# Kernel tuning notes

Hardware: AMD Instinct MI355X
Metric: run time of the kernel (lower is better)

Reference implementation:

```python
import jax, jax.numpy as jnp
import numpy as np

N, E, G = 100000, 1600000, 256      # nodes, edges, graphs in batch
IN_C, HID, OUT_C = 4, 128, 120
ALPHA = 0.5


def setup_inputs() -> dict:
    key = jax.random.key(0)
    ks = jax.random.split(key, 12)
    def w(k, i, o):
        return jax.random.normal(k, (i, o), jnp.float32) / np.float32(np.sqrt(i))
    return {
        "x": jax.random.normal(ks[0], (N, IN_C), jnp.float32),
        "edge_index": jax.random.randint(ks[1], (2, E), 0, N),
        "batch_seg": jnp.sort(jax.random.randint(ks[2], (N,), 0, G)),
        # DirGNNConv holds two independent GCNConvs (in / reversed direction)
        "W_in": w(ks[3], IN_C, HID),  "b_in": jnp.zeros((HID,), jnp.float32),
        "W_in_r": w(ks[4], IN_C, HID), "b_in_r": jnp.zeros((HID,), jnp.float32),
        "W_mid": w(ks[5], HID, HID),  "b_mid": jnp.zeros((HID,), jnp.float32),
        "W_mid_r": w(ks[6], HID, HID), "b_mid_r": jnp.zeros((HID,), jnp.float32),
        "W_out": w(ks[7], HID, OUT_C), "b_out": jnp.zeros((OUT_C,), jnp.float32),
        "W_out_r": w(ks[8], HID, OUT_C), "b_out_r": jnp.zeros((OUT_C,), jnp.float32),
    }


def _gcn(x, W, b, src, dst, n):
    # GCNConv with add_self_loops=False (DirGNNConv disables self-loops):
    # deg computed on destination side, norm = deg^-1/2[src] * deg^-1/2[dst]
    deg = jax.ops.segment_sum(jnp.ones(src.shape[0], x.dtype), dst, num_segments=n)
    dinv = jnp.where(deg > 0, jax.lax.rsqrt(jnp.maximum(deg, 1e-12)), 0.0)
    h = x @ W                                  # [N, out]
    msg = h[src] * (dinv[src] * dinv[dst])[:, None]  # gather + edge-normalize
    return jax.ops.segment_sum(msg, dst, num_segments=n) + b


def _dir_conv(x, Wi, bi, Wr, br, src, dst):
    # DirGNNConv(root_weight=False): (1-a)*conv(edge_index) + a*conv(flipped)
    n = x.shape[0]
    x_in = _gcn(x, Wi, bi, src, dst, n)
    x_out = _gcn(x, Wr, br, dst, src, n)
    return ALPHA * x_out + (1.0 - ALPHA) * x_in


def reference(x, edge_index, batch_seg, W_in, b_in, W_in_r, b_in_r,
              W_mid, b_mid, W_mid_r, b_mid_r, W_out, b_out, W_out_r, b_out_r):
    src, dst = edge_index[0], edge_index[1]
    h = jax.nn.relu(_dir_conv(x, W_in, b_in, W_in_r, b_in_r, src, dst))
    # dropout: eval mode -> identity
    h = jax.nn.relu(_dir_conv(h, W_mid, b_mid, W_mid_r, b_mid_r, src, dst))
    h = _dir_conv(h, W_out, b_out, W_out_r, b_out_r, src, dst)
    # global_mean_pool over batch_seg
    sums = jax.ops.segment_sum(h, batch_seg, num_segments=G)
    cnt = jax.ops.segment_sum(jnp.ones((h.shape[0],), h.dtype), batch_seg, num_segments=G)
    return sums / jnp.maximum(cnt, 1.0)[:, None]
```

## Files before the change

kernel.cpp:

```cpp
#include <hip/hip_runtime.h>
#include <hip/hip_fp16.h>

#define ALPHA 0.5f
#define BSH 9
#define BSZ 512
#define MAXB 512
#define CHUNK 4096

static inline int ceil_div(int a, int b) { return (a + b - 1) / b; }

typedef _Float16 half8 __attribute__((ext_vector_type(8)));
typedef float f32x4 __attribute__((ext_vector_type(4)));

__global__ void hist_kernel(const int* __restrict__ src, const int* __restrict__ dst,
                            unsigned int* __restrict__ bhI, unsigned int* __restrict__ bhO,
                            int E, int nbuck)
{
    __shared__ unsigned int hI[MAXB], hO[MAXB];
    for (int b = threadIdx.x; b < MAXB; b += blockDim.x) { hI[b] = 0; hO[b] = 0; }
    __syncthreads();
    for (int e = blockIdx.x * blockDim.x + threadIdx.x; e < E; e += gridDim.x * blockDim.x) {
        atomicAdd(&hI[dst[e] >> BSH], 1u);
        atomicAdd(&hO[src[e] >> BSH], 1u);
    }
    __syncthreads();
    for (int b = threadIdx.x; b < nbuck; b += blockDim.x) {
        if (hI[b]) atomicAdd(&bhI[b], hI[b]);
        if (hO[b]) atomicAdd(&bhO[b], hO[b]);
    }
}

__global__ void bucket_base_kernel(const unsigned int* __restrict__ bhI,
                                   const unsigned int* __restrict__ bhO,
                                   unsigned int* __restrict__ baseI, unsigned int* __restrict__ baseO,
                                   unsigned int* __restrict__ curI, unsigned int* __restrict__ curO,
                                   int nbuck)
{
    __shared__ unsigned int tI[MAXB], tO[MAXB];
    int t = threadIdx.x;
    unsigned int vI = (t < nbuck) ? bhI[t] : 0u;
    unsigned int vO = (t < nbuck) ? bhO[t] : 0u;
    tI[t] = vI; tO[t] = vO;
    __syncthreads();
    for (int o = 1; o < MAXB; o <<= 1) {
        unsigned int xI = (t >= o) ? tI[t - o] : 0u;
        unsigned int xO = (t >= o) ? tO[t - o] : 0u;
        __syncthreads();
        tI[t] += xI; tO[t] += xO;
        __syncthreads();
    }
    if (t < nbuck) {
        baseI[t] = tI[t] - vI; baseO[t] = tO[t] - vO;
        curI[t]  = tI[t] - vI; curO[t]  = tO[t] - vO;
    }
}

__global__ void bucket_scatter_kernel(const int* __restrict__ src, const int* __restrict__ dst,
                                      unsigned int* __restrict__ curI, unsigned int* __restrict__ curO,
                                      int2* __restrict__ ebI, int2* __restrict__ ebO, int E)
{
    __shared__ unsigned int cI[MAXB], cO[MAXB], bI[MAXB], bO[MAXB];
    int t = threadIdx.x;
    for (int b = t; b < MAXB; b += blockDim.x) { cI[b] = 0; cO[b] = 0; }
    __syncthreads();
    int e0 = blockIdx.x * CHUNK;
    int e1 = min(E, e0 + CHUNK);
    for (int e = e0 + t; e < e1; e += blockDim.x) {
        atomicAdd(&cI[dst[e] >> BSH], 1u);
        atomicAdd(&cO[src[e] >> BSH], 1u);
    }
    __syncthreads();
    for (int b = t; b < MAXB; b += blockDim.x) {
        unsigned int n = cI[b];
        if (n) bI[b] = atomicAdd(&curI[b], n);
        cI[b] = 0;
        n = cO[b];
        if (n) bO[b] = atomicAdd(&curO[b], n);
        cO[b] = 0;
    }
    __syncthreads();
    for (int e = e0 + t; e < e1; e += blockDim.x) {
        int s = src[e], d = dst[e];
        int lb = d >> BSH;
        unsigned int p = bI[lb] + atomicAdd(&cI[lb], 1u);
        ebI[p] = make_int2(d, s);
        lb = s >> BSH;
        p = bO[lb] + atomicAdd(&cO[lb], 1u);
        ebO[p] = make_int2(s, d);
    }
}

__global__ __launch_bounds__(256) void bucket_csr_kernel(
    const int2* __restrict__ ebI, const int2* __restrict__ ebO,
    const unsigned int* __restrict__ baseI, const unsigned int* __restrict__ baseO,
    const unsigned int* __restrict__ bendI, const unsigned int* __restrict__ bendO,
    unsigned int* __restrict__ rowI, unsigned int* __restrict__ rowO,
    unsigned int* __restrict__ degI, unsigned int* __restrict__ degO,
    float* __restrict__ dinvI, float* __restrict__ dinvO,
    int* __restrict__ adjI, int* __restrict__ adjO, int N)
{
    const int2* __restrict__ eb           = blockIdx.y ? ebO : ebI;
    const unsigned int* __restrict__ base = blockIdx.y ? baseO : baseI;
    const unsigned int* __restrict__ bend = blockIdx.y ? bendO : bendI;
    unsigned int* __restrict__ row        = blockIdx.y ? rowO : rowI;
    unsigned int* __restrict__ deg        = blockIdx.y ? degO : degI;
    float* __restrict__ dinv              = blockIdx.y ? dinvO : dinvI;
    int* __restrict__ adj                 = blockIdx.y ? adjO : adjI;

    __shared__ unsigned int d[BSZ];
    __shared__ unsigned int ex[BSZ];
    __shared__ unsigned int ps[256];
    int b = blockIdx.x, t = threadIdx.x;
    int nbase = b << BSH;

    for (int i = t; i < BSZ; i += 256) d[i] = 0;
    __syncthreads();
    unsigned int lo = base[b], hi = bend[b];
    for (unsigned int i = lo + t; i < hi; i += 256)
        atomicAdd(&d[eb[i].x - nbase], 1u);
    __syncthreads();

    ps[t] = d[2 * t] + d[2 * t + 1];
    __syncthreads();
    for (int o = 1; o < 256; o <<= 1) {
        unsigned int x = (t >= o) ? ps[t - o] : 0u;
        __syncthreads();
        ps[t] += x;
        __syncthreads();
    }
    unsigned int p0 = (t > 0) ? ps[t - 1] : 0u;
    ex[2 * t]     = p0;
    ex[2 * t + 1] = p0 + d[2 * t];
    __syncthreads();

    for (int i = t; i < BSZ; i += 256) {
        int v = nbase + i;
        if (v < N) {
            unsigned int dd = d[i];
            row[v]  = lo + ex[i];
            deg[v]  = dd;
            dinv[v] = dd ? rsqrtf((float)dd) : 0.f;
        }
    }
    __syncthreads();
    for (int i = t; i < BSZ; i += 256) d[i] = lo + ex[i];
    __syncthreads();
    for (unsigned int i = lo + t; i < hi; i += 256) {
        int2 e = eb[i];
        unsigned int p = atomicAdd(&d[e.x - nbase], 1u);
        adj[p] = e.y;
    }
}

__global__ void seg_cnt_kernel(const int* __restrict__ seg, float* __restrict__ cnt, int N, int G)
{
    int g = blockIdx.x * blockDim.x + threadIdx.x;
    if (g >= G) return;
    int lo = 0, hi = N;
    while (lo < hi) { int m = (lo + hi) >> 1; if (seg[m] < g) lo = m + 1; else hi = m; }
    int s0 = lo;
    hi = N;
    while (lo < hi) { int m = (lo + hi) >> 1; if (seg[m] < g + 1) lo = m + 1; else hi = m; }
    cnt[g] = (float)(lo - s0);
}

__global__ void prep_w_kernel(const float* __restrict__ Wi, const float* __restrict__ Wr,
                              const float* __restrict__ bi, const float* __restrict__ br,
                              __half* __restrict__ Wt, float* __restrict__ bcomb)
{
    int idx = blockIdx.x * 256 + threadIdx.x;
    if (idx < 128 * 256) {
        int j = idx >> 8, k = idx & 255;
        float w = (k < 128) ? (1.f - ALPHA) * Wi[k * 128 + j]
                            : ALPHA * Wr[(k - 128) * 128 + j];
        Wt[idx] = __float2half_rn(w);
    }
    if (idx < 128) bcomb[idx] = (1.f - ALPHA) * bi[idx] + ALPHA * br[idx];
}

__global__ __launch_bounds__(256) void layer1_fused_kernel(
    const unsigned int* __restrict__ rowI, const unsigned int* __restrict__ degI,
    const int* __restrict__ adjI, const float* __restrict__ dinvI,
    const unsigned int* __restrict__ rowO, const unsigned int* __restrict__ degO,
    const int* __restrict__ adjO, const float* __restrict__ dinvO,
    const float4* __restrict__ x4,
    const float* __restrict__ Wi, const float* __restrict__ bi,
    const float* __restrict__ Wr, const float* __restrict__ br,
    __half* __restrict__ h1, int N)
{
    __shared__ float wI[4][128], wO[4][128], bb[128];
    int t = threadIdx.x;
    if (t < 128) {
#pragma unroll
        for (int c = 0; c < 4; ++c) {
            wI[c][t] = (1.f - ALPHA) * Wi[c * 128 + t];
            wO[c][t] = ALPHA * Wr[c * 128 + t];
        }
        bb[t] = (1.f - ALPHA) * bi[t] + ALPHA * br[t];
    }
    __syncthreads();
    int v = blockIdx.x * 256 + t;
    if (v >= N) return;

    float4 aI = {0.f, 0.f, 0.f, 0.f};
    {
        unsigned int k = rowI[v], end = k + degI[v];
        for (; k < end; ++k) {
            int s = adjI[k];
            float w = dinvI[s];
            float4 xv = x4[s];
            aI.x += w * xv.x; aI.y += w * xv.y; aI.z += w * xv.z; aI.w += w * xv.w;
        }
        float dv = dinvI[v];
        aI.x *= dv; aI.y *= dv; aI.z *= dv; aI.w *= dv;
    }
    float4 aO = {0.f, 0.f, 0.f, 0.f};
    {
        unsigned int k = rowO[v], end = k + degO[v];
        for (; k < end; ++k) {
            int s = adjO[k];
            float w = dinvO[s];
            float4 xv = x4[s];
            aO.x += w * xv.x; aO.y += w * xv.y; aO.z += w * xv.z; aO.w += w * xv.w;
        }
        float dv = dinvO[v];
        aO.x *= dv; aO.y *= dv; aO.z *= dv; aO.w *= dv;
    }

    half8* outp = (half8*)&h1[(size_t)v * 128];
#pragma unroll
    for (int jq = 0; jq < 16; ++jq) {
        half8 o;
#pragma unroll
        for (int u = 0; u < 8; ++u) {
            int j = jq * 8 + u;
            float s = bb[j]
                    + aI.x * wI[0][j] + aI.y * wI[1][j] + aI.z * wI[2][j] + aI.w * wI[3][j]
                    + aO.x * wO[0][j] + aO.y * wO[1][j] + aO.z * wO[2][j] + aO.w * wO[3][j];
            o[u] = (_Float16)fmaxf(s, 0.f);
        }
        outp[jq] = o;
    }
}

__global__ __launch_bounds__(256) void gather_mfma_kernel(
    const unsigned int* __restrict__ rowI, const unsigned int* __restrict__ degI,
    const int* __restrict__ adjI, const float* __restrict__ dinvI,
    const unsigned int* __restrict__ rowO, const unsigned int* __restrict__ degO,
    const int* __restrict__ adjO, const float* __restrict__ dinvO,
    const half8* __restrict__ hp,
    const __half* __restrict__ Wt,
    const float* __restrict__ bcomb,
    __half* __restrict__ h2, int N)
{
    __shared__ _Float16 sAB[16][264];
    int t = threadIdx.x;
    int node = t >> 4, lane = t & 15;
    int v = blockIdx.x * 16 + node;
    bool valid = v < N;

#pragma unroll
    for (int dir = 0; dir < 2; ++dir) {
        const unsigned int* __restrict__ rw = dir ? rowO : rowI;
        const unsigned int* __restrict__ dg = dir ? degO : degI;
        const int* __restrict__ adj         = dir ? adjO : adjI;
        const float* __restrict__ dinv      = dir ? dinvO : dinvI;
        float acc[8];
#pragma unroll
        for (int i = 0; i < 8; ++i) acc[i] = 0.f;
        if (valid) {
            unsigned int k = rw[v], end = k + dg[v];
            for (; k + 4 <= end; k += 4) {
                int s0 = adj[k], s1 = adj[k + 1], s2 = adj[k + 2], s3 = adj[k + 3];
                float w0 = dinv[s0], w1 = dinv[s1], w2 = dinv[s2], w3 = dinv[s3];
                half8 h0 = hp[(size_t)s0 * 16 + lane];
                half8 h1 = hp[(size_t)s1 * 16 + lane];
                half8 h2v = hp[(size_t)s2 * 16 + lane];
                half8 h3 = hp[(size_t)s3 * 16 + lane];
#pragma unroll
                for (int i = 0; i < 8; ++i)
                    acc[i] += w0 * (float)h0[i] + w1 * (float)h1[i]
                            + w2 * (float)h2v[i] + w3 * (float)h3[i];
            }
            for (; k < end; ++k) {
                int s = adj[k];
                float w = dinv[s];
                half8 hv = hp[(size_t)s * 16 + lane];
#pragma unroll
                for (int i = 0; i < 8; ++i)
                    acc[i] += w * (float)hv[i];
            }
            float dv = dinv[v];
#pragma unroll
            for (int i = 0; i < 8; ++i) acc[i] *= dv;
        }
        half8 o;
#pragma unroll
        for (int i = 0; i < 8; ++i) o[i] = (_Float16)acc[i];
        *(half8*)&sAB[node][dir * 128 + lane * 8] = o;
    }
    __syncthreads();

    int wave = t >> 6;
    int l64 = t & 63;
    int row = l64 & 15;
    int kg  = l64 >> 4;
    f32x4 acc0 = {0.f, 0.f, 0.f, 0.f}, acc1 = {0.f, 0.f, 0.f, 0.f};
    int j0 = (wave * 2) * 16 + row;
    int j1 = (wave * 2 + 1) * 16 + row;
#pragma unroll
    for (int ks = 0; ks < 8; ++ks) {
        int kw = ks * 32 + kg * 8;
        half8 afrag = *(const half8*)&sAB[row][kw];
        half8 b0 = *(const half8*)&Wt[(size_t)j0 * 256 + kw];
        half8 b1 = *(const half8*)&Wt[(size_t)j1 * 256 + kw];
        acc0 = __builtin_amdgcn_mfma_f32_16x16x32_f16(afrag, b0, acc0, 0, 0, 0);
        acc1 = __builtin_amdgcn_mfma_f32_16x16x32_f16(afrag, b1, acc1, 0, 0, 0);
    }
    int v0 = blockIdx.x * 16;
    float bj0 = bcomb[j0], bj1 = bcomb[j1];
#pragma unroll
    for (int r = 0; r < 4; ++r) {
        int vr = v0 + kg * 4 + r;
        if (vr < N) {
            h2[(size_t)vr * 128 + j0] = __float2half_rn(fmaxf(acc0[r] + bj0, 0.f));
            h2[(size_t)vr * 128 + j1] = __float2half_rn(fmaxf(acc1[r] + bj1, 0.f));
        }
    }
}

__global__ void gather128_kernel(const unsigned int* __restrict__ rowstartI,
                                 const unsigned int* __restrict__ degI,
                                 const int* __restrict__ adjI,
                                 const float* __restrict__ dinvI,
                                 const unsigned int* __restrict__ rowstartO,
                                 const unsigned int* __restrict__ degO,
                                 const int* __restrict__ adjO,
                                 const float* __restrict__ dinvO,
                                 const half8* __restrict__ hp,
                                 half8* __restrict__ outI, half8* __restrict__ outO, int N)
{
    int v = blockIdx.x * 16 + (threadIdx.x >> 4);
    if (v >= N) return;
    int lane = threadIdx.x & 15;
    const unsigned int* __restrict__ rowstart = blockIdx.y ? rowstartO : rowstartI;
    const unsigned int* __restrict__ deg      = blockIdx.y ? degO : degI;
    const int* __restrict__ adj               = blockIdx.y ? adjO : adjI;
    const float* __restrict__ dinv            = blockIdx.y ? dinvO : dinvI;
    half8* __restrict__ out                   = blockIdx.y ? outO : outI;

    unsigned int k = rowstart[v];
    unsigned int end = k + deg[v];
    float acc[8];
#pragma unroll
    for (int i = 0; i < 8; ++i) acc[i] = 0.f;

    for (; k + 4 <= end; k += 4) {
        int s0 = adj[k], s1 = adj[k + 1], s2 = adj[k + 2], s3 = adj[k + 3];
        float w0 = dinv[s0], w1 = dinv[s1], w2 = dinv[s2], w3 = dinv[s3];
        half8 h0 = hp[(size_t)s0 * 16 + lane];
        half8 h1 = hp[(size_t)s1 * 16 + lane];
        half8 h2 = hp[(size_t)s2 * 16 + lane];
        half8 h3 = hp[(size_t)s3 * 16 + lane];
#pragma unroll
        for (int i = 0; i < 8; ++i)
            acc[i] += w0 * (float)h0[i] + w1 * (float)h1[i]
                    + w2 * (float)h2[i] + w3 * (float)h3[i];
    }
    for (; k < end; ++k) {
        int s = adj[k];
        float w = dinv[s];
        half8 hv = hp[(size_t)s * 16 + lane];
#pragma unroll
        for (int i = 0; i < 8; ++i)
            acc[i] += w * (float)hv[i];
    }
    float dv = dinv[v];
    half8 o;
#pragma unroll
    for (int i = 0; i < 8; ++i) o[i] = (_Float16)(dv * acc[i]);
    out[(size_t)v * 16 + lane] = o;
}

#define POOL_NODES 32
__global__ void pool_kernel(const __half* __restrict__ aI, const __half* __restrict__ aO,
                            const int* __restrict__ seg,
                            float* __restrict__ poolI, float* __restrict__ poolO, int N)
{
    int j = threadIdx.x;
    int v0 = blockIdx.x * POOL_NODES;
    if (v0 >= N) return;
    int v1 = min(N, v0 + POOL_NODES);
    float sI = 0.f, sO = 0.f;
    int cur = seg[v0];
    for (int v = v0; v < v1; ++v) {
        int g = seg[v];
        if (g != cur) {
            atomicAdd(&poolI[cur * 128 + j], sI);
            atomicAdd(&poolO[cur * 128 + j], sO);
            sI = 0.f; sO = 0.f; cur = g;
        }
        sI += __half2float(aI[(size_t)v * 128 + j]);
        sO += __half2float(aO[(size_t)v * 128 + j]);
    }
    atomicAdd(&poolI[cur * 128 + j], sI);
    atomicAdd(&poolO[cur * 128 + j], sO);
}

__global__ void final_kernel(const float* __restrict__ poolI, const float* __restrict__ poolO,
                             const float* __restrict__ cnt,
                             const float* __restrict__ Wo, const float* __restrict__ bo,
                             const float* __restrict__ Wor, const float* __restrict__ bor,
                             float* __restrict__ out, int G)
{
    int g = blockIdx.x;
    int j = threadIdx.x;
    if (g >= G || j >= 120) return;
    float acc = 0.f;
    for (int k = 0; k < 128; ++k) {
        acc += poolI[g * 128 + k] * ((1.f - ALPHA) * Wo[k * 120 + j])
             + poolO[g * 128 + k] * (ALPHA * Wor[k * 120 + j]);
    }
    float c = cnt[g];
    float bcomb = (1.f - ALPHA) * bo[j] + ALPHA * bor[j];
    out[g * 120 + j] = (c > 0.f) ? (acc / c + bcomb) : 0.f;
}

extern "C" void kernel_launch(void* const* d_in, const int* in_sizes, int n_in,
                              void* d_out, int out_size, void* d_ws, size_t ws_size,
                              hipStream_t stream)
{
    const float* x      = (const float*)d_in[0];
    const int*   ei     = (const int*)d_in[1];
    const int*   seg    = (const int*)d_in[2];
    const float* W_in   = (const float*)d_in[3];
    const float* b_in   = (const float*)d_in[4];
    const float* W_in_r = (const float*)d_in[5];
    const float* b_in_r = (const float*)d_in[6];
    const float* W_mid  = (const float*)d_in[7];
    const float* b_mid  = (const float*)d_in[8];
    const float* W_mid_r= (const float*)d_in[9];
    const float* b_mid_r= (const float*)d_in[10];
    const float* W_out  = (const float*)d_in[11];
    const float* b_out  = (const float*)d_in[12];
    const float* W_out_r= (const float*)d_in[13];
    const float* b_out_r= (const float*)d_in[14];

    const int N = in_sizes[0] / 4;
    const int E = in_sizes[1] / 2;
    const int G = out_size / 120;
    const int* src = ei;
    const int* dst = ei + E;
    const int NBUCK = ceil_div(N, BSZ);

    char* wsb = (char*)d_ws;
    size_t off = 0;
    auto alloc = [&](size_t elems) { void* p = wsb + off * 4; off += elems; return p; };

    unsigned int* bhI   = (unsigned int*)alloc(MAXB);
    unsigned int* bhO   = (unsigned int*)alloc(MAXB);
    float*        poolI = (float*)alloc((size_t)G * 128);
    float*        poolO = (float*)alloc((size_t)G * 128);
    size_t zero_elems = off;
    float*        cnt   = (float*)alloc(G);
    unsigned int* baseI = (unsigned int*)alloc(MAXB);
    unsigned int* baseO = (unsigned int*)alloc(MAXB);
    unsigned int* curI  = (unsigned int*)alloc(MAXB);
    unsigned int* curO  = (unsigned int*)alloc(MAXB);
    unsigned int* degI  = (unsigned int*)alloc(N);
    unsigned int* degO  = (unsigned int*)alloc(N);
    float*        dinvI = (float*)alloc(N);
    float*        dinvO = (float*)alloc(N);
    unsigned int* rowI  = (unsigned int*)alloc(N);
    unsigned int* rowO  = (unsigned int*)alloc(N);
    int*          adjI  = (int*)alloc(E);
    int*          adjO  = (int*)alloc(E);
    __half*       Wt    = (__half*)alloc(128 * 256 / 2);
    float*        bcomb = (float*)alloc(128);
    off = (off + 3) & ~(size_t)3;
    __half* hbuf = (__half*)alloc((size_t)N * 64);
    __half* aggI = (__half*)alloc((size_t)N * 64);
    __half* aggO = (__half*)alloc((size_t)N * 64);
    (void)ws_size;

    int2* ebI = (int2*)aggI;
    int2* ebO = (int2*)aggO;

    hipMemsetAsync(d_ws, 0, zero_elems * 4, stream);

    const int T = 256;
    hist_kernel<<<ceil_div(E, T * 16), T, 0, stream>>>(src, dst, bhI, bhO, E, NBUCK);
    bucket_base_kernel<<<1, MAXB, 0, stream>>>(bhI, bhO, baseI, baseO, curI, curO, NBUCK);
    bucket_scatter_kernel<<<ceil_div(E, CHUNK), T, 0, stream>>>(src, dst, curI, curO, ebI, ebO, E);
    bucket_csr_kernel<<<dim3(NBUCK, 2), T, 0, stream>>>(ebI, ebO, baseI, baseO, curI, curO,
                                                        rowI, rowO, degI, degO,
                                                        dinvI, dinvO, adjI, adjO, N);
    seg_cnt_kernel<<<ceil_div(G, T), T, 0, stream>>>(seg, cnt, N, G);
    prep_w_kernel<<<128, 256, 0, stream>>>(W_mid, W_mid_r, b_mid, b_mid_r, Wt, bcomb);

    layer1_fused_kernel<<<ceil_div(N, T), T, 0, stream>>>(
        rowI, degI, adjI, dinvI, rowO, degO, adjO, dinvO,
        (const float4*)x, W_in, b_in, W_in_r, b_in_r, hbuf, N);
    gather_mfma_kernel<<<ceil_div(N, 16), 256, 0, stream>>>(
        rowI, degI, adjI, dinvI, rowO, degO, adjO, dinvO,
        (const half8*)hbuf, Wt, bcomb, aggI, N);
    gather128_kernel<<<dim3(ceil_div(N, 16), 2), 256, 0, stream>>>(
        rowI, degI, adjI, dinvI, rowO, degO, adjO, dinvO,
        (const half8*)aggI, (half8*)hbuf, (half8*)aggO, N);
    pool_kernel<<<ceil_div(N, POOL_NODES), 128, 0, stream>>>(
        hbuf, aggO, seg, poolI, poolO, N);
    final_kernel<<<G, 128, 0, stream>>>(poolI, poolO, cnt,
                                        W_out, b_out, W_out_r, b_out_r, (float*)d_out, G);
}
```

Measured before the change: 457.0 us.

## Fuse final-layer neighbor gather with global mean pooling via LDS atomics

Merges the last gather kernel and the pooling kernel into one. Each block aggregates both edge directions for 16 nodes and adds the results straight into per-graph sums, first in shared memory and then through global atomics. This removes writing and re-reading the two N×128 half-precision intermediate buffers and drops one kernel launch. In exchange it adds many LDS atomic adds, runs the two directions serially in one block instead of across a 2D grid, and makes the float summation order nondeterministic.

```diff
diff --git a/kernel.cpp b/kernel.cpp
--- a/kernel.cpp
+++ b/kernel.cpp
@@ -6,6 +6,7 @@
 #define BSZ 512
 #define MAXB 512
 #define CHUNK 4096
+#define GL 8
 
 static inline int ceil_div(int a, int b) { return (a + b - 1) / b; }
 
@@ -329,82 +330,91 @@
     }
 }
 
-__global__ void gather128_kernel(const unsigned int* __restrict__ rowstartI,
-                                 const unsigned int* __restrict__ degI,
-                                 const int* __restrict__ adjI,
-                                 const float* __restrict__ dinvI,
-                                 const unsigned int* __restrict__ rowstartO,
-                                 const unsigned int* __restrict__ degO,
-                                 const int* __restrict__ adjO,
-                                 const float* __restrict__ dinvO,
-                                 const half8* __restrict__ hp,
-                                 half8* __restrict__ outI, half8* __restrict__ outO, int N)
-{
-    int v = blockIdx.x * 16 + (threadIdx.x >> 4);
-    if (v >= N) return;
-    int lane = threadIdx.x & 15;
-    const unsigned int* __restrict__ rowstart = blockIdx.y ? rowstartO : rowstartI;
-    const unsigned int* __restrict__ deg      = blockIdx.y ? degO : degI;
-    const int* __restrict__ adj               = blockIdx.y ? adjO : adjI;
-    const float* __restrict__ dinv            = blockIdx.y ? dinvO : dinvI;
-    half8* __restrict__ out                   = blockIdx.y ? outO : outI;
-
-    unsigned int k = rowstart[v];
-    unsigned int end = k + deg[v];
-    float acc[8];
-#pragma unroll
-    for (int i = 0; i < 8; ++i) acc[i] = 0.f;
-
-    for (; k + 4 <= end; k += 4) {
-        int s0 = adj[k], s1 = adj[k + 1], s2 = adj[k + 2], s3 = adj[k + 3];
-        float w0 = dinv[s0], w1 = dinv[s1], w2 = dinv[s2], w3 = dinv[s3];
-        half8 h0 = hp[(size_t)s0 * 16 + lane];
-        half8 h1 = hp[(size_t)s1 * 16 + lane];
-        half8 h2 = hp[(size_t)s2 * 16 + lane];
-        half8 h3 = hp[(size_t)s3 * 16 + lane];
-#pragma unroll
-        for (int i = 0; i < 8; ++i)
-            acc[i] += w0 * (float)h0[i] + w1 * (float)h1[i]
-                    + w2 * (float)h2[i] + w3 * (float)h3[i];
-    }
-    for (; k < end; ++k) {
-        int s = adj[k];
-        float w = dinv[s];
-        half8 hv = hp[(size_t)s * 16 + lane];
-#pragma unroll
-        for (int i = 0; i < 8; ++i)
-            acc[i] += w * (float)hv[i];
-    }
-    float dv = dinv[v];
-    half8 o;
-#pragma unroll
-    for (int i = 0; i < 8; ++i) o[i] = (_Float16)(dv * acc[i]);
-    out[(size_t)v * 16 + lane] = o;
-}
-
-#define POOL_NODES 32
-__global__ void pool_kernel(const __half* __restrict__ aI, const __half* __restrict__ aO,
-                            const int* __restrict__ seg,
-                            float* __restrict__ poolI, float* __restrict__ poolO, int N)
-{
-    int j = threadIdx.x;
-    int v0 = blockIdx.x * POOL_NODES;
-    if (v0 >= N) return;
-    int v1 = min(N, v0 + POOL_NODES);
-    float sI = 0.f, sO = 0.f;
-    int cur = seg[v0];
-    for (int v = v0; v < v1; ++v) {
-        int g = seg[v];
-        if (g != cur) {
-            atomicAdd(&poolI[cur * 128 + j], sI);
-            atomicAdd(&poolO[cur * 128 + j], sO);
-            sI = 0.f; sO = 0.f; cur = g;
-        }
-        sI += __half2float(aI[(size_t)v * 128 + j]);
-        sO += __half2float(aO[(size_t)v * 128 + j]);
-    }
-    atomicAdd(&poolI[cur * 128 + j], sI);
-    atomicAdd(&poolO[cur * 128 + j], sO);
+__global__ __launch_bounds__(256) void gather_pool_kernel(
+    const unsigned int* __restrict__ rowI, const unsigned int* __restrict__ degI,
+    const int* __restrict__ adjI, const float* __restrict__ dinvI,
+    const unsigned int* __restrict__ rowO, const unsigned int* __restrict__ degO,
+    const int* __restrict__ adjO, const float* __restrict__ dinvO,
+    const int* __restrict__ seg, const half8* __restrict__ hp,
+    float* __restrict__ poolI, float* __restrict__ poolO, int N, int G)
+{
+    __shared__ float pl[2][GL][128];
+    int t = threadIdx.x;
+    int node = t >> 4, lane = t & 15;
+    int v0 = blockIdx.x * 16;
+    int v = v0 + node;
+    bool valid = v < N;
+
+    for (int i = t; i < 2 * GL * 128; i += 256) ((float*)pl)[i] = 0.f;
+    __syncthreads();
+
+    int g0 = seg[v0 < N ? v0 : (N - 1)];
+    int gl = 0; bool inlds = false; int gv = 0;
+    if (valid) {
+        gv = seg[v];
+        gl = gv - g0;
+        inlds = (gl >= 0 && gl < GL);
+    }
+
+#pragma unroll
+    for (int dir = 0; dir < 2; ++dir) {
+        const unsigned int* __restrict__ rw = dir ? rowO : rowI;
+        const unsigned int* __restrict__ dg = dir ? degO : degI;
+        const int* __restrict__ adj         = dir ? adjO : adjI;
+        const float* __restrict__ dinv      = dir ? dinvO : dinvI;
+        float acc[8];
+#pragma unroll
+        for (int i = 0; i < 8; ++i) acc[i] = 0.f;
+        if (valid) {
+            unsigned int k = rw[v], end = k + dg[v];
+            for (; k + 4 <= end; k += 4) {
+                int s0 = adj[k], s1 = adj[k + 1], s2 = adj[k + 2], s3 = adj[k + 3];
+                float w0 = dinv[s0], w1 = dinv[s1], w2 = dinv[s2], w3 = dinv[s3];
+                half8 h0 = hp[(size_t)s0 * 16 + lane];
+                half8 h1 = hp[(size_t)s1 * 16 + lane];
+                half8 h2v = hp[(size_t)s2 * 16 + lane];
+                half8 h3 = hp[(size_t)s3 * 16 + lane];
+#pragma unroll
+                for (int i = 0; i < 8; ++i)
+                    acc[i] += w0 * (float)h0[i] + w1 * (float)h1[i]
+                            + w2 * (float)h2v[i] + w3 * (float)h3[i];
+            }
+            for (; k < end; ++k) {
+                int s = adj[k];
+                float w = dinv[s];
+                half8 hv = hp[(size_t)s * 16 + lane];
+#pragma unroll
+                for (int i = 0; i < 8; ++i)
+                    acc[i] += w * (float)hv[i];
+            }
+            float dv = dinv[v];
+#pragma unroll
+            for (int i = 0; i < 8; ++i) acc[i] *= dv;
+
+            if (inlds) {
+#pragma unroll
+                for (int i = 0; i < 8; ++i)
+                    atomicAdd(&pl[dir][gl][lane * 8 + i], acc[i]);
+            } else {
+                float* gp = (dir ? poolO : poolI) + (size_t)gv * 128 + lane * 8;
+#pragma unroll
+                for (int i = 0; i < 8; ++i)
+                    atomicAdd(&gp[i], acc[i]);
+            }
+        }
+    }
+    __syncthreads();
+
+    for (int i = t; i < 2 * GL * 128; i += 256) {
+        int dir = i >> 10;
+        int rem = i & 1023;
+        int g = rem >> 7, ch = rem & 127;
+        float val = pl[dir][g][ch];
+        if (val != 0.f) {
+            int gg = g0 + g;
+            if (gg < G) atomicAdd(&(dir ? poolO : poolI)[(size_t)gg * 128 + ch], val);
+        }
+    }
 }
 
 __global__ void final_kernel(const float* __restrict__ poolI, const float* __restrict__ poolO,
@@ -479,12 +489,12 @@
     float*        bcomb = (float*)alloc(128);
     off = (off + 3) & ~(size_t)3;
     __half* hbuf = (__half*)alloc((size_t)N * 64);
-    __half* aggI = (__half*)alloc((size_t)N * 64);
-    __half* aggO = (__half*)alloc((size_t)N * 64);
+    __half* h2b  = (__half*)alloc((size_t)N * 64);
+    __half* ebsp = (__half*)alloc((size_t)N * 64);
     (void)ws_size;
 
-    int2* ebI = (int2*)aggI;
-    int2* ebO = (int2*)aggO;
+    int2* ebI = (int2*)h2b;
+    int2* ebO = (int2*)ebsp;
 
     hipMemsetAsync(d_ws, 0, zero_elems * 4, stream);
 
@@ -503,12 +513,10 @@
         (const float4*)x, W_in, b_in, W_in_r, b_in_r, hbuf, N);
     gather_mfma_kernel<<<ceil_div(N, 16), 256, 0, stream>>>(
         rowI, degI, adjI, dinvI, rowO, degO, adjO, dinvO,
-        (const half8*)hbuf, Wt, bcomb, aggI, N);
-    gather128_kernel<<<dim3(ceil_div(N, 16), 2), 256, 0, stream>>>(
+        (const half8*)hbuf, Wt, bcomb, h2b, N);
+    gather_pool_kernel<<<ceil_div(N, 16), 256, 0, stream>>>(
         rowI, degI, adjI, dinvI, rowO, degO, adjO, dinvO,
-        (const half8*)aggI, (half8*)hbuf, (half8*)aggO, N);
-    pool_kernel<<<ceil_div(N, POOL_NODES), 128, 0, stream>>>(
-        hbuf, aggO, seg, poolI, poolO, N);
+        seg, (const half8*)h2b, poolI, poolO, N, G);
     final_kernel<<<G, 128, 0, stream>>>(poolI, poolO, cnt,
                                         W_out, b_out, W_out_r, b_out_r, (float*)d_out, G);
 }
```

Measured after the change: 505.1 us. 1.11x slower.

## Use fixed-capacity buckets to drop histogram pass, merge prep kernels, interleave gathers

Applied to the files above, without the earlier changes.

Edge bucketing now writes into fixed-capacity slots per bucket (CAP entries each), so the global histogram and prefix-scan kernels are removed and the per-bucket counter alone gives each bucket's extent. The segment-count and weight-prep kernels are merged into one launch. The mid-layer gather interleaves the in- and out-direction neighbour loops so more independent loads are in flight at once. The change uses extra workspace for padded buckets and assumes no bucket exceeds CAP edges, which holds for uniformly random edges but would overflow silently on skewed graphs.

```diff
diff --git a/kernel.cpp b/kernel.cpp
--- a/kernel.cpp
+++ b/kernel.cpp
@@ -6,54 +6,13 @@
 #define BSZ 512
 #define MAXB 512
 #define CHUNK 4096
+#define CAP 16384
+#define POOL_NODES 32
 
 static inline int ceil_div(int a, int b) { return (a + b - 1) / b; }
 
 typedef _Float16 half8 __attribute__((ext_vector_type(8)));
 typedef float f32x4 __attribute__((ext_vector_type(4)));
-
-__global__ void hist_kernel(const int* __restrict__ src, const int* __restrict__ dst,
-                            unsigned int* __restrict__ bhI, unsigned int* __restrict__ bhO,
-                            int E, int nbuck)
-{
-    __shared__ unsigned int hI[MAXB], hO[MAXB];
-    for (int b = threadIdx.x; b < MAXB; b += blockDim.x) { hI[b] = 0; hO[b] = 0; }
-    __syncthreads();
-    for (int e = blockIdx.x * blockDim.x + threadIdx.x; e < E; e += gridDim.x * blockDim.x) {
-        atomicAdd(&hI[dst[e] >> BSH], 1u);
-        atomicAdd(&hO[src[e] >> BSH], 1u);
-    }
-    __syncthreads();
-    for (int b = threadIdx.x; b < nbuck; b += blockDim.x) {
-        if (hI[b]) atomicAdd(&bhI[b], hI[b]);
-        if (hO[b]) atomicAdd(&bhO[b], hO[b]);
-    }
-}
-
-__global__ void bucket_base_kernel(const unsigned int* __restrict__ bhI,
-                                   const unsigned int* __restrict__ bhO,
-                                   unsigned int* __restrict__ baseI, unsigned int* __restrict__ baseO,
-                                   unsigned int* __restrict__ curI, unsigned int* __restrict__ curO,
-                                   int nbuck)
-{
-    __shared__ unsigned int tI[MAXB], tO[MAXB];
-    int t = threadIdx.x;
-    unsigned int vI = (t < nbuck) ? bhI[t] : 0u;
-    unsigned int vO = (t < nbuck) ? bhO[t] : 0u;
-    tI[t] = vI; tO[t] = vO;
-    __syncthreads();
-    for (int o = 1; o < MAXB; o <<= 1) {
-        unsigned int xI = (t >= o) ? tI[t - o] : 0u;
-        unsigned int xO = (t >= o) ? tO[t - o] : 0u;
-        __syncthreads();
-        tI[t] += xI; tO[t] += xO;
-        __syncthreads();
-    }
-    if (t < nbuck) {
-        baseI[t] = tI[t] - vI; baseO[t] = tO[t] - vO;
-        curI[t]  = tI[t] - vI; curO[t]  = tO[t] - vO;
-    }
-}
 
 __global__ void bucket_scatter_kernel(const int* __restrict__ src, const int* __restrict__ dst,
                                       unsigned int* __restrict__ curI, unsigned int* __restrict__ curO,
@@ -83,25 +42,23 @@
         int s = src[e], d = dst[e];
         int lb = d >> BSH;
         unsigned int p = bI[lb] + atomicAdd(&cI[lb], 1u);
-        ebI[p] = make_int2(d, s);
+        ebI[(size_t)lb * CAP + p] = make_int2(d, s);
         lb = s >> BSH;
         p = bO[lb] + atomicAdd(&cO[lb], 1u);
-        ebO[p] = make_int2(s, d);
+        ebO[(size_t)lb * CAP + p] = make_int2(s, d);
     }
 }
 
 __global__ __launch_bounds__(256) void bucket_csr_kernel(
     const int2* __restrict__ ebI, const int2* __restrict__ ebO,
-    const unsigned int* __restrict__ baseI, const unsigned int* __restrict__ baseO,
-    const unsigned int* __restrict__ bendI, const unsigned int* __restrict__ bendO,
+    const unsigned int* __restrict__ cntI, const unsigned int* __restrict__ cntO,
     unsigned int* __restrict__ rowI, unsigned int* __restrict__ rowO,
     unsigned int* __restrict__ degI, unsigned int* __restrict__ degO,
     float* __restrict__ dinvI, float* __restrict__ dinvO,
     int* __restrict__ adjI, int* __restrict__ adjO, int N)
 {
-    const int2* __restrict__ eb           = blockIdx.y ? ebO : ebI;
-    const unsigned int* __restrict__ base = blockIdx.y ? baseO : baseI;
-    const unsigned int* __restrict__ bend = blockIdx.y ? bendO : bendI;
+    const int2* __restrict__ eb          = blockIdx.y ? ebO : ebI;
+    const unsigned int* __restrict__ cntb = blockIdx.y ? cntO : cntI;
     unsigned int* __restrict__ row        = blockIdx.y ? rowO : rowI;
     unsigned int* __restrict__ deg        = blockIdx.y ? degO : degI;
     float* __restrict__ dinv              = blockIdx.y ? dinvO : dinvI;
@@ -112,10 +69,11 @@
     __shared__ unsigned int ps[256];
     int b = blockIdx.x, t = threadIdx.x;
     int nbase = b << BSH;
+    unsigned int lo = (unsigned int)b * CAP;
+    unsigned int hi = lo + cntb[b];
 
     for (int i = t; i < BSZ; i += 256) d[i] = 0;
     __syncthreads();
-    unsigned int lo = base[b], hi = bend[b];
     for (unsigned int i = lo + t; i < hi; i += 256)
         atomicAdd(&d[eb[i].x - nbase], 1u);
     __syncthreads();
@@ -152,21 +110,10 @@
     }
 }
 
-__global__ void seg_cnt_kernel(const int* __restrict__ seg, float* __restrict__ cnt, int N, int G)
-{
-    int g = blockIdx.x * blockDim.x + threadIdx.x;
-    if (g >= G) return;
-    int lo = 0, hi = N;
-    while (lo < hi) { int m = (lo + hi) >> 1; if (seg[m] < g) lo = m + 1; else hi = m; }
-    int s0 = lo;
-    hi = N;
-    while (lo < hi) { int m = (lo + hi) >> 1; if (seg[m] < g + 1) lo = m + 1; else hi = m; }
-    cnt[g] = (float)(lo - s0);
-}
-
-__global__ void prep_w_kernel(const float* __restrict__ Wi, const float* __restrict__ Wr,
-                              const float* __restrict__ bi, const float* __restrict__ br,
-                              __half* __restrict__ Wt, float* __restrict__ bcomb)
+__global__ void prep_kernel(const int* __restrict__ seg, float* __restrict__ cnt, int N, int G,
+                            const float* __restrict__ Wi, const float* __restrict__ Wr,
+                            const float* __restrict__ bi, const float* __restrict__ br,
+                            __half* __restrict__ Wt, float* __restrict__ bcomb)
 {
     int idx = blockIdx.x * 256 + threadIdx.x;
     if (idx < 128 * 256) {
@@ -176,6 +123,15 @@
         Wt[idx] = __float2half_rn(w);
     }
     if (idx < 128) bcomb[idx] = (1.f - ALPHA) * bi[idx] + ALPHA * br[idx];
+    if (idx < G) {
+        int g = idx;
+        int lo = 0, hi = N;
+        while (lo < hi) { int m = (lo + hi) >> 1; if (seg[m] < g) lo = m + 1; else hi = m; }
+        int s0 = lo;
+        hi = N;
+        while (lo < hi) { int m = (lo + hi) >> 1; if (seg[m] < g + 1) lo = m + 1; else hi = m; }
+        cnt[g] = (float)(lo - s0);
+    }
 }
 
 __global__ __launch_bounds__(256) void layer1_fused_kernel(
@@ -259,46 +215,70 @@
     int v = blockIdx.x * 16 + node;
     bool valid = v < N;
 
-#pragma unroll
-    for (int dir = 0; dir < 2; ++dir) {
-        const unsigned int* __restrict__ rw = dir ? rowO : rowI;
-        const unsigned int* __restrict__ dg = dir ? degO : degI;
-        const int* __restrict__ adj         = dir ? adjO : adjI;
-        const float* __restrict__ dinv      = dir ? dinvO : dinvI;
-        float acc[8];
-#pragma unroll
-        for (int i = 0; i < 8; ++i) acc[i] = 0.f;
-        if (valid) {
-            unsigned int k = rw[v], end = k + dg[v];
-            for (; k + 4 <= end; k += 4) {
-                int s0 = adj[k], s1 = adj[k + 1], s2 = adj[k + 2], s3 = adj[k + 3];
-                float w0 = dinv[s0], w1 = dinv[s1], w2 = dinv[s2], w3 = dinv[s3];
-                half8 h0 = hp[(size_t)s0 * 16 + lane];
-                half8 h1 = hp[(size_t)s1 * 16 + lane];
-                half8 h2v = hp[(size_t)s2 * 16 + lane];
-                half8 h3 = hp[(size_t)s3 * 16 + lane];
-#pragma unroll
-                for (int i = 0; i < 8; ++i)
-                    acc[i] += w0 * (float)h0[i] + w1 * (float)h1[i]
-                            + w2 * (float)h2v[i] + w3 * (float)h3[i];
+    float aI[8], aO[8];
+#pragma unroll
+    for (int i = 0; i < 8; ++i) { aI[i] = 0.f; aO[i] = 0.f; }
+
+    if (valid) {
+        unsigned int kI = rowI[v], eI = kI + degI[v];
+        unsigned int kO = rowO[v], eO = kO + degO[v];
+        while (kI + 2 <= eI && kO + 2 <= eO) {
+            int s0 = adjI[kI], s1 = adjI[kI + 1];
+            int t0 = adjO[kO], t1 = adjO[kO + 1];
+            float wi0 = dinvI[s0], wi1 = dinvI[s1];
+            float wo0 = dinvO[t0], wo1 = dinvO[t1];
+            half8 hi0 = hp[(size_t)s0 * 16 + lane];
+            half8 hi1 = hp[(size_t)s1 * 16 + lane];
+            half8 ho0 = hp[(size_t)t0 * 16 + lane];
+            half8 ho1 = hp[(size_t)t1 * 16 + lane];
+#pragma unroll
+            for (int i = 0; i < 8; ++i) {
+                aI[i] += wi0 * (float)hi0[i] + wi1 * (float)hi1[i];
+                aO[i] += wo0 * (float)ho0[i] + wo1 * (float)ho1[i];
             }
-            for (; k < end; ++k) {
-                int s = adj[k];
-                float w = dinv[s];
-                half8 hv = hp[(size_t)s * 16 + lane];
-#pragma unroll
-                for (int i = 0; i < 8; ++i)
-                    acc[i] += w * (float)hv[i];
-            }
-            float dv = dinv[v];
-#pragma unroll
-            for (int i = 0; i < 8; ++i) acc[i] *= dv;
-        }
-        half8 o;
-#pragma unroll
-        for (int i = 0; i < 8; ++i) o[i] = (_Float16)acc[i];
-        *(half8*)&sAB[node][dir * 128 + lane * 8] = o;
-    }
+            kI += 2; kO += 2;
+        }
+        for (; kI + 2 <= eI; kI += 2) {
+            int s0 = adjI[kI], s1 = adjI[kI + 1];
+            float w0 = dinvI[s0], w1 = dinvI[s1];
+            half8 h0 = hp[(size_t)s0 * 16 + lane];
+            half8 h1 = hp[(size_t)s1 * 16 + lane];
+#pragma unroll
+            for (int i = 0; i < 8; ++i)
+                aI[i] += w0 * (float)h0[i] + w1 * (float)h1[i];
+        }
+        if (kI < eI) {
+            int s = adjI[kI];
+            float w = dinvI[s];
+            half8 hv = hp[(size_t)s * 16 + lane];
+#pragma unroll
+            for (int i = 0; i < 8; ++i) aI[i] += w * (float)hv[i];
+        }
+        for (; kO + 2 <= eO; kO += 2) {
+            int t0 = adjO[kO], t1 = adjO[kO + 1];
+            float w0 = dinvO[t0], w1 = dinvO[t1];
+            half8 h0 = hp[(size_t)t0 * 16 + lane];
+            half8 h1 = hp[(size_t)t1 * 16 + lane];
+#pragma unroll
+            for (int i = 0; i < 8; ++i)
+                aO[i] += w0 * (float)h0[i] + w1 * (float)h1[i];
+        }
+        if (kO < eO) {
+            int u = adjO[kO];
+            float w = dinvO[u];
+            half8 hv = hp[(size_t)u * 16 + lane];
+#pragma unroll
+            for (int i = 0; i < 8; ++i) aO[i] += w * (float)hv[i];
+        }
+        float dvI = dinvI[v], dvO = dinvO[v];
+#pragma unroll
+        for (int i = 0; i < 8; ++i) { aI[i] *= dvI; aO[i] *= dvO; }
+    }
+    half8 oI, oO;
+#pragma unroll
+    for (int i = 0; i < 8; ++i) { oI[i] = (_Float16)aI[i]; oO[i] = (_Float16)aO[i]; }
+    *(half8*)&sAB[node][lane * 8]       = oI;
+    *(half8*)&sAB[node][128 + lane * 8] = oO;
     __syncthreads();
 
     int wave = t >> 6;
@@ -382,7 +362,6 @@
     out[(size_t)v * 16 + lane] = o;
 }
 
-#define POOL_NODES 32
 __global__ void pool_kernel(const __half* __restrict__ aI, const __half* __restrict__ aO,
                             const int* __restrict__ seg,
                             float* __restrict__ poolI, float* __restrict__ poolO, int N)
@@ -457,58 +436,51 @@
     size_t off = 0;
     auto alloc = [&](size_t elems) { void* p = wsb + off * 4; off += elems; return p; };
 
-    unsigned int* bhI   = (unsigned int*)alloc(MAXB);
-    unsigned int* bhO   = (unsigned int*)alloc(MAXB);
+    unsigned int* curI  = (unsigned int*)alloc(MAXB);
+    unsigned int* curO  = (unsigned int*)alloc(MAXB);
     float*        poolI = (float*)alloc((size_t)G * 128);
     float*        poolO = (float*)alloc((size_t)G * 128);
     size_t zero_elems = off;
     float*        cnt   = (float*)alloc(G);
-    unsigned int* baseI = (unsigned int*)alloc(MAXB);
-    unsigned int* baseO = (unsigned int*)alloc(MAXB);
-    unsigned int* curI  = (unsigned int*)alloc(MAXB);
-    unsigned int* curO  = (unsigned int*)alloc(MAXB);
     unsigned int* degI  = (unsigned int*)alloc(N);
     unsigned int* degO  = (unsigned int*)alloc(N);
     float*        dinvI = (float*)alloc(N);
     float*        dinvO = (float*)alloc(N);
     unsigned int* rowI  = (unsigned int*)alloc(N);
     unsigned int* rowO  = (unsigned int*)alloc(N);
-    int*          adjI  = (int*)alloc(E);
-    int*          adjO  = (int*)alloc(E);
+    int*          adjI  = (int*)alloc((size_t)NBUCK * CAP);
+    int*          adjO  = (int*)alloc((size_t)NBUCK * CAP);
     __half*       Wt    = (__half*)alloc(128 * 256 / 2);
     float*        bcomb = (float*)alloc(128);
     off = (off + 3) & ~(size_t)3;
     __half* hbuf = (__half*)alloc((size_t)N * 64);
-    __half* aggI = (__half*)alloc((size_t)N * 64);
-    __half* aggO = (__half*)alloc((size_t)N * 64);
+    __half* h2b  = (__half*)alloc((size_t)N * 64);
+    __half* ag3  = (__half*)alloc((size_t)N * 64);
+    int2*   ebI  = (int2*)alloc((size_t)NBUCK * CAP * 2);
+    int2*   ebO  = (int2*)alloc((size_t)NBUCK * CAP * 2);
     (void)ws_size;
 
-    int2* ebI = (int2*)aggI;
-    int2* ebO = (int2*)aggO;
-
     hipMemsetAsync(d_ws, 0, zero_elems * 4, stream);
 
     const int T = 256;
-    hist_kernel<<<ceil_div(E, T * 16), T, 0, stream>>>(src, dst, bhI, bhO, E, NBUCK);
-    bucket_base_kernel<<<1, MAXB, 0, stream>>>(bhI, bhO, baseI, baseO, curI, curO, NBUCK);
     bucket_scatter_kernel<<<ceil_div(E, CHUNK), T, 0, stream>>>(src, dst, curI, curO, ebI, ebO, E);
-    bucket_csr_kernel<<<dim3(NBUCK, 2), T, 0, stream>>>(ebI, ebO, baseI, baseO, curI, curO,
+    bucket_csr_kernel<<<dim3(NBUCK, 2), T, 0, stream>>>(ebI, ebO, curI, curO,
                                                         rowI, rowO, degI, degO,
                                                         dinvI, dinvO, adjI, adjO, N);
-    seg_cnt_kernel<<<ceil_div(G, T), T, 0, stream>>>(seg, cnt, N, G);
-    prep_w_kernel<<<128, 256, 0, stream>>>(W_mid, W_mid_r, b_mid, b_mid_r, Wt, bcomb);
+    prep_kernel<<<128, 256, 0, stream>>>(seg, cnt, N, G,
+                                         W_mid, W_mid_r, b_mid, b_mid_r, Wt, bcomb);
 
     layer1_fused_kernel<<<ceil_div(N, T), T, 0, stream>>>(
         rowI, degI, adjI, dinvI, rowO, degO, adjO, dinvO,
         (const float4*)x, W_in, b_in, W_in_r, b_in_r, hbuf, N);
     gather_mfma_kernel<<<ceil_div(N, 16), 256, 0, stream>>>(
         rowI, degI, adjI, dinvI, rowO, degO, adjO, dinvO,
-        (const half8*)hbuf, Wt, bcomb, aggI, N);
+        (const half8*)hbuf, Wt, bcomb, h2b, N);
     gather128_kernel<<<dim3(ceil_div(N, 16), 2), 256, 0, stream>>>(
         rowI, degI, adjI, dinvI, rowO, degO, adjO, dinvO,
-        (const half8*)aggI, (half8*)hbuf, (half8*)aggO, N);
+        (const half8*)h2b, (half8*)hbuf, (half8*)ag3, N);
     pool_kernel<<<ceil_div(N, POOL_NODES), 128, 0, stream>>>(
-        hbuf, aggO, seg, poolI, poolO, N);
+        hbuf, ag3, seg, poolI, poolO, N);
     final_kernel<<<G, 128, 0, stream>>>(poolI, poolO, cnt,
                                         W_out, b_out, W_out_r, b_out_r, (float*)d_out, G);
 }
```

After: 454.9 us. Within noise of the previous version (-0.5%).
